# Kernel tuning notes

Measured on AMD Instinct MI355X. Metric: run time of the kernel, lower is better.

## Reference

```python
import jax, jax.numpy as jnp
import numpy as np

N = 50000          # nodes
E = 800000         # edges
IN = 32            # in_channels (train_tensor.shape[1])
OUT = 256          # out_channels
K = 4              # Chebyshev order
LAMBDA_MAX = 2.0   # canonical lambda_max for sym-normalized Laplacian


def setup_inputs() -> dict:
    key = jax.random.key(0)
    ks = jax.random.split(key, 32)
    inp = {}
    inp["X"] = jax.random.normal(ks[0], (N, IN), jnp.float32)
    inp["edge_index"] = jax.random.randint(ks[1], (2, E), 0, N)
    inp["edge_weight"] = jax.random.uniform(ks[2], (E,), jnp.float32)
    inp["H"] = jax.random.normal(ks[3], (N, OUT), jnp.float32)
    inp["C"] = jax.random.normal(ks[4], (N, OUT), jnp.float32)
    i = 5
    s_in = float(np.sqrt(6.0 / (IN + OUT)))   # glorot for W_g
    s_ch = float(np.sqrt(1.0 / OUT))          # ChebConv linear init scale
    for g in ["i", "f", "c", "o"]:
        inp[f"W_{g}"] = jax.random.uniform(ks[i], (IN, OUT), jnp.float32, -s_in, s_in); i += 1
        inp[f"b_{g}"] = jnp.zeros((1, OUT), jnp.float32)
        inp[f"conv_{g}_w"] = jax.random.uniform(ks[i], (K, OUT, OUT), jnp.float32, -s_ch, s_ch); i += 1
        inp[f"conv_{g}_b"] = jnp.zeros((OUT,), jnp.float32)
    return inp


def _cheb_basis(H, edge_index, edge_weight, lam):
    """Chebyshev basis T_0(L~)H .. T_{K-1}(L~)H for the scaled sym Laplacian.
    L~ = (2/lam) * (I - D^{-1/2} A D^{-1/2}) - I  (PyG ChebConv.__norm__)."""
    n = H.shape[0]
    src, dst = edge_index[0], edge_index[1]
    deg = jax.ops.segment_sum(edge_weight, src, num_segments=n)
    dis = jnp.where(deg > 0, jax.lax.rsqrt(deg), 0.0)
    w = -(2.0 / lam) * dis[src] * edge_weight * dis[dst]   # scaled off-diagonal
    d = 2.0 / lam - 1.0                                     # scaled diagonal

    def prop(x):  # L~ @ x via edge scatter + diagonal
        return jax.ops.segment_sum(w[:, None] * x[src], dst, num_segments=n) + d * x

    Tx0 = H
    Tx1 = prop(Tx0)
    Tx2 = 2.0 * prop(Tx1) - Tx0
    Tx3 = 2.0 * prop(Tx2) - Tx1
    return jnp.stack([Tx0, Tx1, Tx2, Tx3])  # [K, N, OUT]


def reference(X, edge_index, edge_weight, H, C,
              W_i, b_i, conv_i_w, conv_i_b,
              W_f, b_f, conv_f_w, conv_f_b,
              W_c, b_c, conv_c_w, conv_c_b,
              W_o, b_o, conv_o_w, conv_o_b):
    # Shared Chebyshev basis of H (identical across the 4 gates)
    Tx = _cheb_basis(H, edge_index, edge_weight, LAMBDA_MAX)  # [K, N, OUT]

    def gate(Wg, bg, cw, cb):
        conv = jnp.einsum('knf,kfo->no', Tx, cw) + cb
        return X @ Wg + conv + bg

    I = jax.nn.sigmoid(gate(W_i, b_i, conv_i_w, conv_i_b))
    F = jax.nn.sigmoid(gate(W_f, b_f, conv_f_w, conv_f_b))
    T = jnp.tanh(gate(W_c, b_c, conv_c_w, conv_c_b))
    C_new = F * C + I * T
    O = jax.nn.sigmoid(gate(W_o, b_o, conv_o_w, conv_o_b))
    H_new = O * jnp.tanh(C_new)
    return (H_new, C_new)
```

## Files before the change

kernel.cpp:

```cpp
#include <hip/hip_runtime.h>
#include <math.h>

#define NN   50000
#define EE   800000
#define INC  32
#define OUTC 256
#define NKB  132

using bf16x8 = __attribute__((ext_vector_type(8))) short;
using u16x8  = __attribute__((ext_vector_type(8))) unsigned short;
using f32x4  = __attribute__((ext_vector_type(4))) float;

struct __align__(8) Edge { int s; float w; };

__device__ __forceinline__ unsigned short f2b(float f) {
  union { float f; unsigned u; } v; v.f = f;
  return (unsigned short)((v.u + 0x7FFFu + ((v.u >> 16) & 1u)) >> 16);
}
__device__ __forceinline__ float b2f(unsigned short u) {
  union { unsigned u; float f; } v; v.u = ((unsigned)u) << 16; return v.f;
}


__global__ void k_edge1(const int* __restrict__ ei, const float* __restrict__ ew,
                        float* __restrict__ deg, int* __restrict__ cnt) {
  for (int e = blockIdx.x * blockDim.x + threadIdx.x; e < EE;
       e += gridDim.x * blockDim.x) {
    atomicAdd(&deg[ei[e]], ew[e]);
    atomicAdd(&cnt[ei[EE + e]], 1);
  }
}

__global__ __launch_bounds__(512) void k_scan1(const int* __restrict__ cnt,
                                               int* __restrict__ row_ptr,
                                               int* __restrict__ bsum) {
  __shared__ int sd[512];
  int t = threadIdx.x;
  int i = blockIdx.x * 512 + t;
  int x = (i < NN) ? cnt[i] : 0;
  sd[t] = x;
  __syncthreads();
  for (int off = 1; off < 512; off <<= 1) {
    int v = (t >= off) ? sd[t - off] : 0;
    __syncthreads();
    sd[t] += v;
    __syncthreads();
  }
  if (i < NN) row_ptr[i] = sd[t] - x;
  if (t == 511) bsum[blockIdx.x] = sd[511];
}

__global__ __launch_bounds__(128) void k_scan2(int* __restrict__ bsum,
                                               int* __restrict__ row_ptr,
                                               int nblk) {
  __shared__ int sd[128];
  int t = threadIdx.x;
  int x = (t < nblk) ? bsum[t] : 0;
  sd[t] = x;
  __syncthreads();
  for (int off = 1; off < 128; off <<= 1) {
    int v = (t >= off) ? sd[t - off] : 0;
    __syncthreads();
    sd[t] += v;
    __syncthreads();
  }
  if (t < nblk) bsum[t] = sd[t] - x;
  if (t == 127) row_ptr[NN] = sd[127];
}

__global__ void k_scan3(int* __restrict__ row_ptr, const int* __restrict__ bsum,
                        int* __restrict__ nxt, float* __restrict__ deg) {
  int i = blockIdx.x * blockDim.x + threadIdx.x;
  if (i < NN) {
    int v = row_ptr[i] + bsum[i >> 9];
    row_ptr[i] = v;
    nxt[i] = v;
    float d = deg[i];
    deg[i] = d > 0.f ? rsqrtf(d) : 0.f;
  }
}

__global__ void k_fill(const int* __restrict__ ei, const float* __restrict__ ew,
                       const float* __restrict__ dis, int* __restrict__ nxt,
                       Edge* __restrict__ ev) {
  for (int e = blockIdx.x * blockDim.x + threadIdx.x; e < EE;
       e += gridDim.x * blockDim.x) {
    int s = ei[e], d = ei[EE + e];
    int pos = atomicAdd(&nxt[d], 1);
    Edge eg; eg.s = s; eg.w = -dis[s] * ew[e] * dis[d];
    ev[pos] = eg;
  }
}


__global__ __launch_bounds__(256) void k_prop_bf(
    const int* __restrict__ row_ptr, const Edge* __restrict__ ev,
    const unsigned short* __restrict__ xb,
    const unsigned short* __restrict__ initb, float scale,
    unsigned short* __restrict__ outb, unsigned short* __restrict__ apk) {
  int wid = blockIdx.x * 4 + (threadIdx.x >> 6);
  if (wid >= NN) return;
  int lane = threadIdx.x & 63;
  int half = lane >> 5;
  int cl = lane & 31;
  int start = __builtin_amdgcn_readfirstlane(row_ptr[wid]);
  int end = __builtin_amdgcn_readfirstlane(row_ptr[wid + 1]);
  const size_t cofs = (size_t)(cl << 3);

  float a0[8], a1[8], a2[8], a3[8];
#pragma unroll
  for (int i = 0; i < 8; ++i) { a0[i] = 0.f; a1[i] = 0.f; a2[i] = 0.f; a3[i] = 0.f; }

  int j = start;
  for (; j + 7 < end; j += 8) {
    Edge e0 = ev[j + half];
    Edge e1 = ev[j + 2 + half];
    Edge e2 = ev[j + 4 + half];
    Edge e3 = ev[j + 6 + half];
    u16x8 u0 = *(const u16x8*)(xb + (size_t)e0.s * OUTC + cofs);
    u16x8 u1 = *(const u16x8*)(xb + (size_t)e1.s * OUTC + cofs);
    u16x8 u2 = *(const u16x8*)(xb + (size_t)e2.s * OUTC + cofs);
    u16x8 u3 = *(const u16x8*)(xb + (size_t)e3.s * OUTC + cofs);
#pragma unroll
    for (int i = 0; i < 8; ++i) {
      a0[i] = fmaf(e0.w, b2f(u0[i]), a0[i]);
      a1[i] = fmaf(e1.w, b2f(u1[i]), a1[i]);
      a2[i] = fmaf(e2.w, b2f(u2[i]), a2[i]);
      a3[i] = fmaf(e3.w, b2f(u3[i]), a3[i]);
    }
  }
  for (; j + 1 < end; j += 2) {
    Edge e0 = ev[j + half];
    u16x8 u0 = *(const u16x8*)(xb + (size_t)e0.s * OUTC + cofs);
#pragma unroll
    for (int i = 0; i < 8; ++i) a0[i] = fmaf(e0.w, b2f(u0[i]), a0[i]);
  }
  if (j < end) {
    Edge e0 = ev[j];
    float wv = half ? 0.f : e0.w;
    u16x8 u0 = *(const u16x8*)(xb + (size_t)e0.s * OUTC + cofs);
#pragma unroll
    for (int i = 0; i < 8; ++i) a0[i] = fmaf(wv, b2f(u0[i]), a0[i]);
  }

  float o[8];
#pragma unroll
  for (int i = 0; i < 8; ++i) {
    float s = (a0[i] + a1[i]) + (a2[i] + a3[i]);
    s += __shfl_xor(s, 32);
    o[i] = s;
  }
  if (initb) {
    u16x8 iv = *(const u16x8*)(initb + (size_t)wid * OUTC + cofs);
#pragma unroll
    for (int i = 0; i < 8; ++i) o[i] = scale * o[i] - b2f(iv[i]);
  }
  u16x8 h;
#pragma unroll
  for (int i = 0; i < 8; ++i) h[i] = f2b(o[i]);
  if (half == 0) {
    *(u16x8*)(apk + ((size_t)cl * NN + wid) * 8) = h;
  } else if (outb) {
    *(u16x8*)(outb + (size_t)wid * OUTC + cofs) = h;
  }
}


__global__ void k_packXH(const float* __restrict__ X, const float* __restrict__ H,
                         unsigned short* __restrict__ apk,
                         unsigned short* __restrict__ hrm) {
  int t = blockIdx.x * blockDim.x + threadIdx.x;
  if (t < NN * 4) {
    int row = t >> 2, kb = t & 3;
    float4 a = *(const float4*)(X + (size_t)row * INC + kb * 8);
    float4 b = *(const float4*)(X + (size_t)row * INC + kb * 8 + 4);
    u16x8 h;
    h[0] = f2b(a.x); h[1] = f2b(a.y); h[2] = f2b(a.z); h[3] = f2b(a.w);
    h[4] = f2b(b.x); h[5] = f2b(b.y); h[6] = f2b(b.z); h[7] = f2b(b.w);
    *(u16x8*)(apk + ((size_t)kb * NN + row) * 8) = h;
  } else if (t < NN * 36) {
    int u = t - NN * 4;
    int row = u >> 5, kb = u & 31;
    float4 a = *(const float4*)(H + (size_t)row * OUTC + kb * 8);
    float4 b = *(const float4*)(H + (size_t)row * OUTC + kb * 8 + 4);
    u16x8 h;
    h[0] = f2b(a.x); h[1] = f2b(a.y); h[2] = f2b(a.z); h[3] = f2b(a.w);
    h[4] = f2b(b.x); h[5] = f2b(b.y); h[6] = f2b(b.z); h[7] = f2b(b.w);
    *(u16x8*)(apk + ((size_t)(kb + 4) * NN + row) * 8) = h;
    *(u16x8*)(hrm + (size_t)row * OUTC + kb * 8) = h;
  }
}

struct BPtrs {
  const float* W[4];
  const float* cw[4];
  const float* b[4];
  const float* cb[4];
};

__global__ void k_packB(BPtrs bp, unsigned short* __restrict__ bpk,
                        float* __restrict__ bias_pk) {
  int t = blockIdx.x * blockDim.x + threadIdx.x;
  if (t >= NKB * 1024) return;
  int kb = t >> 10, p = t & 1023;
  int j = p >> 7, c = (p >> 6) & 1, g = (p >> 4) & 3, s = p & 15;
  int o = j * 32 + c * 16 + s;
  u16x8 h;
#pragma unroll
  for (int j8 = 0; j8 < 8; ++j8) {
    int k = kb * 8 + j8;
    float v = (k < 32) ? bp.W[g][k * OUTC + o]
                       : bp.cw[g][(size_t)(k - 32) * OUTC + o];
    h[j8] = f2b(v);
  }
  *(u16x8*)(bpk + (size_t)t * 8) = h;
  if (kb == 0) bias_pk[p] = bp.b[g][o] + bp.cb[g][o];
}


__device__ __forceinline__ float sigf(float x) {
  return __builtin_amdgcn_rcpf(1.0f + __expf(-x));
}
__device__ __forceinline__ float tanhfast(float x) {
  float e = __expf(2.0f * x);
  return 1.0f - 2.0f * __builtin_amdgcn_rcpf(e + 1.0f);
}

#define AS1(p) ((__attribute__((address_space(1))) void*)(p))
#define AS3(p) ((__attribute__((address_space(3))) void*)(p))

__global__ __launch_bounds__(512, 6) void k_gemm_mfma(
    const unsigned short* __restrict__ Apk,
    const unsigned short* __restrict__ Bpk,
    const float* __restrict__ bias_pk,
    const float* __restrict__ C,
    float* __restrict__ Hn, float* __restrict__ Cn) {
  __shared__ unsigned short Als[3][4 * 128 * 8];
  __shared__ unsigned short Bls[3][4 * 128 * 8];

  const int b = blockIdx.x;
  const int xcd = b & 7;
  const int slot = b >> 3;
  const int cgrp = slot & 7;
  const int rblk = xcd + ((slot >> 3) << 3);
  const int bm0 = rblk * 128;
  if (bm0 >= NN) return;
  const int cb0 = cgrp * 128;

  const int tid = threadIdx.x;
  const int lane = tid & 63;
  const int wid = tid >> 6;
  const int wr = wid >> 1;
  const int wc = wid & 1;

  f32x4 acc[2][4];
#pragma unroll
  for (int i = 0; i < 2; ++i)
#pragma unroll
    for (int j = 0; j < 4; ++j) acc[i][j] = (f32x4){0.f, 0.f, 0.f, 0.f};

  int a_row = bm0 + ((wid & 1) << 6) + lane;
  if (a_row > NN - 1) a_row = NN - 1;
  const unsigned short* aG = Apk + ((size_t)(wid >> 1) * NN + a_row) * 8;
  const int idxw = wid << 6;
  const unsigned short* bG =
      Bpk + (((size_t)(idxw >> 7)) * 1024 + cb0 + (idxw & 127) + lane) * 8;

  auto STAGE_A = [&](int buf, int tile) {
    __builtin_amdgcn_global_load_lds(AS1(aG + ((size_t)(tile << 2)) * NN * 8),
                                     AS3(&Als[buf][(wid << 6) * 8]), 16, 0, 0);
  };
  auto STAGE_B = [&](int buf, int tile) {
    __builtin_amdgcn_global_load_lds(AS1(bG + ((size_t)(tile << 2)) * 1024 * 8),
                                     AS3(&Bls[buf][(wid << 6) * 8]), 16, 0, 0);
  };

  const int koff = lane >> 4;
  const int r15 = lane & 15;
  const int NT = NKB / 4;

  STAGE_A(0, 0); STAGE_B(0, 0);
  STAGE_A(1, 1); STAGE_B(1, 1);
  int cur = 0;
  for (int t = 0; t < NT; ++t) {
    if (t < NT - 1)
      asm volatile("s_waitcnt vmcnt(2)\n\ts_barrier" ::: "memory");
    else
      asm volatile("s_waitcnt vmcnt(0)\n\ts_barrier" ::: "memory");

    const unsigned short* Ab = &Als[cur][((koff << 7) + (wr << 5) + r15) * 8];
    const unsigned short* Bb = &Bls[cur][((koff << 7) + (wc << 6) + r15) * 8];

    bf16x8 af0 = *(const bf16x8*)(Ab + 0 * 8);
    bf16x8 af1 = *(const bf16x8*)(Ab + 16 * 8);
    bf16x8 bf0 = *(const bf16x8*)(Bb + 0 * 8);
    bf16x8 bf1 = *(const bf16x8*)(Bb + 16 * 8);
    bf16x8 bf2 = *(const bf16x8*)(Bb + 32 * 8);
    bf16x8 bf3 = *(const bf16x8*)(Bb + 48 * 8);
    if (t + 2 < NT) { STAGE_A((t + 2) % 3, t + 2); STAGE_B((t + 2) % 3, t + 2); }
    __builtin_amdgcn_s_barrier();
    asm volatile("s_waitcnt lgkmcnt(0)" ::: "memory");
    __builtin_amdgcn_sched_barrier(0);
    __builtin_amdgcn_s_setprio(1);
    acc[0][0] = __builtin_amdgcn_mfma_f32_16x16x32_bf16(af0, bf0, acc[0][0], 0, 0, 0);
    acc[1][0] = __builtin_amdgcn_mfma_f32_16x16x32_bf16(af1, bf0, acc[1][0], 0, 0, 0);
    acc[0][1] = __builtin_amdgcn_mfma_f32_16x16x32_bf16(af0, bf1, acc[0][1], 0, 0, 0);
    acc[1][1] = __builtin_amdgcn_mfma_f32_16x16x32_bf16(af1, bf1, acc[1][1], 0, 0, 0);
    acc[0][2] = __builtin_amdgcn_mfma_f32_16x16x32_bf16(af0, bf2, acc[0][2], 0, 0, 0);
    acc[1][2] = __builtin_amdgcn_mfma_f32_16x16x32_bf16(af1, bf2, acc[1][2], 0, 0, 0);
    acc[0][3] = __builtin_amdgcn_mfma_f32_16x16x32_bf16(af0, bf3, acc[0][3], 0, 0, 0);
    acc[1][3] = __builtin_amdgcn_mfma_f32_16x16x32_bf16(af1, bf3, acc[1][3], 0, 0, 0);
    __builtin_amdgcn_s_setprio(0);

    cur = (cur + 1 == 3) ? 0 : cur + 1;
  }

  const int ocol = cgrp * 32 + (wc << 4) + r15;
  float bz[4];
#pragma unroll
  for (int g = 0; g < 4; ++g) bz[g] = bias_pk[cb0 + (wc << 6) + (g << 4) + r15];

#pragma unroll
  for (int mi = 0; mi < 2; ++mi) {
    int rowb = bm0 + (wr << 5) + (mi << 4) + ((lane >> 4) << 2);
#pragma unroll
    for (int q = 0; q < 4; ++q) {
      int r = rowb + q;
      if (r >= NN) continue;
      float zi = acc[mi][0][q] + bz[0];
      float zf = acc[mi][1][q] + bz[1];
      float zc = acc[mi][2][q] + bz[2];
      float zo = acc[mi][3][q] + bz[3];
      float cold = C[(size_t)r * OUTC + ocol];
      float I = sigf(zi), F = sigf(zf), T = tanhfast(zc), O = sigf(zo);
      float cn = fmaf(F, cold, I * T);
      Cn[(size_t)r * OUTC + ocol] = cn;
      Hn[(size_t)r * OUTC + ocol] = O * tanhfast(cn);
    }
  }
}


extern "C" void kernel_launch(void* const* d_in, const int* in_sizes, int n_in,
                              void* d_out, int out_size, void* d_ws, size_t ws_size,
                              hipStream_t stream) {
  const float* X = (const float*)d_in[0];
  const int* EI = (const int*)d_in[1];
  const float* EW = (const float*)d_in[2];
  const float* H = (const float*)d_in[3];
  const float* C = (const float*)d_in[4];

  char* ws = (char*)d_ws;
  size_t off = 0;
  auto alloc = [&](size_t bytes) -> void* {
    void* p = ws + off;
    off += (bytes + 255) & ~(size_t)255;
    return p;
  };
  int* row_ptr = (int*)alloc((NN + 1) * sizeof(int));
  int* cnt = (int*)alloc(NN * sizeof(int));
  int* nextp = (int*)alloc(NN * sizeof(int));
  int* bsum = (int*)alloc(128 * sizeof(int));
  Edge* ev = (Edge*)alloc(EE * sizeof(Edge));
  float* dis = (float*)alloc(NN * sizeof(float));
  unsigned short* Hrm = (unsigned short*)alloc((size_t)NN * OUTC * sizeof(unsigned short));
  unsigned short* T1rm = (unsigned short*)alloc((size_t)NN * OUTC * sizeof(unsigned short));
  unsigned short* T2rm = (unsigned short*)alloc((size_t)NN * OUTC * sizeof(unsigned short));
  unsigned short* Apk = (unsigned short*)alloc((size_t)NKB * NN * 8 * sizeof(unsigned short));
  unsigned short* Bpk = (unsigned short*)alloc((size_t)NKB * 1024 * 8 * sizeof(unsigned short));
  float* bias_pk = (float*)alloc(1024 * sizeof(float));
  (void)ws_size; (void)in_sizes; (void)n_in; (void)out_size;

  hipMemsetAsync(dis, 0, NN * sizeof(float), stream);
  hipMemsetAsync(cnt, 0, NN * sizeof(int), stream);

  const int ge = 1024;
  k_edge1<<<ge, 256, 0, stream>>>(EI, EW, dis, cnt);
  const int nscb = (NN + 511) / 512;
  k_scan1<<<nscb, 512, 0, stream>>>(cnt, row_ptr, bsum);
  k_scan2<<<1, 128, 0, stream>>>(bsum, row_ptr, nscb);
  k_scan3<<<(NN + 255) / 256, 256, 0, stream>>>(row_ptr, bsum, nextp, dis);
  k_fill<<<ge, 256, 0, stream>>>(EI, EW, dis, nextp, ev);

  k_packXH<<<(NN * 36 + 255) / 256, 256, 0, stream>>>(X, H, Apk, Hrm);
  BPtrs bp;
  for (int g = 0; g < 4; ++g) {
    bp.W[g] = (const float*)d_in[5 + 4 * g];
    bp.b[g] = (const float*)d_in[6 + 4 * g];
    bp.cw[g] = (const float*)d_in[7 + 4 * g];
    bp.cb[g] = (const float*)d_in[8 + 4 * g];
  }
  k_packB<<<(NKB * 1024 + 255) / 256, 256, 0, stream>>>(bp, Bpk, bias_pk);

  const int pgrid = (NN + 3) / 4;
  k_prop_bf<<<pgrid, 256, 0, stream>>>(row_ptr, ev, Hrm, nullptr, 1.f,
                                       T1rm, Apk + (size_t)36 * NN * 8);
  k_prop_bf<<<pgrid, 256, 0, stream>>>(row_ptr, ev, T1rm, Hrm, 2.f,
                                       T2rm, Apk + (size_t)68 * NN * 8);
  k_prop_bf<<<pgrid, 256, 0, stream>>>(row_ptr, ev, T2rm, T1rm, 2.f,
                                       nullptr, Apk + (size_t)100 * NN * 8);

  float* Hn = (float*)d_out;
  float* Cn = (float*)d_out + (size_t)NN * OUTC;
  k_gemm_mfma<<<8 * 49 * 8, 512, 0, stream>>>(Apk, Bpk, bias_pk, C, Hn, Cn);
}
```

Baseline: 495.4 us.

## Enlarge GEMM block tile to 128x256 with 4 waves and 4x8 MFMA accumulators

Restructures the fused gate GEMM so each 256-thread block computes a 128-row by 256-column tile, with each wave holding a 64x128 output (4x8 MFMA accumulators) instead of 32x64. Column groups drop from 8 to 4 per row block, so the A operand is re-read from global memory half as often and each LDS fragment feeds more MFMAs. The cost is many more accumulator registers per thread, lower occupancy (launch bounds 256,2), a larger LDS B buffer, and more loads in flight per stage, with vmcnt adjusted to match.

```diff
diff --git a/kernel.cpp b/kernel.cpp
--- a/kernel.cpp
+++ b/kernel.cpp
@@ -229,23 +229,23 @@
 #define AS1(p) ((__attribute__((address_space(1))) void*)(p))
 #define AS3(p) ((__attribute__((address_space(3))) void*)(p))
 
-__global__ __launch_bounds__(512, 6) void k_gemm_mfma(
+__global__ __launch_bounds__(256, 2) void k_gemm_mfma(
     const unsigned short* __restrict__ Apk,
     const unsigned short* __restrict__ Bpk,
     const float* __restrict__ bias_pk,
     const float* __restrict__ C,
     float* __restrict__ Hn, float* __restrict__ Cn) {
   __shared__ unsigned short Als[3][4 * 128 * 8];
-  __shared__ unsigned short Bls[3][4 * 128 * 8];
+  __shared__ unsigned short Bls[3][4 * 256 * 8];
 
   const int b = blockIdx.x;
   const int xcd = b & 7;
   const int slot = b >> 3;
-  const int cgrp = slot & 7;
-  const int rblk = xcd + ((slot >> 3) << 3);
+  const int cgrp = slot & 3;
+  const int rblk = xcd + ((slot >> 2) << 3);
   const int bm0 = rblk * 128;
   if (bm0 >= NN) return;
-  const int cb0 = cgrp * 128;
+  const int cb0 = cgrp * 256;
 
   const int tid = threadIdx.x;
   const int lane = tid & 63;
@@ -253,26 +253,32 @@
   const int wr = wid >> 1;
   const int wc = wid & 1;
 
-  f32x4 acc[2][4];
-#pragma unroll
-  for (int i = 0; i < 2; ++i)
-#pragma unroll
-    for (int j = 0; j < 4; ++j) acc[i][j] = (f32x4){0.f, 0.f, 0.f, 0.f};
+  f32x4 acc[4][8];
+#pragma unroll
+  for (int i = 0; i < 4; ++i)
+#pragma unroll
+    for (int j = 0; j < 8; ++j) acc[i][j] = (f32x4){0.f, 0.f, 0.f, 0.f};
 
   int a_row = bm0 + ((wid & 1) << 6) + lane;
   if (a_row > NN - 1) a_row = NN - 1;
-  const unsigned short* aG = Apk + ((size_t)(wid >> 1) * NN + a_row) * 8;
-  const int idxw = wid << 6;
-  const unsigned short* bG =
-      Bpk + (((size_t)(idxw >> 7)) * 1024 + cb0 + (idxw & 127) + lane) * 8;
+  const unsigned short* aG0 = Apk + ((size_t)(wid >> 1) * NN + a_row) * 8;
+  const unsigned short* aG1 = Apk + ((size_t)((wid >> 1) + 2) * NN + a_row) * 8;
+  const unsigned short* bG = Bpk + ((size_t)cb0 + (wid << 6) + lane) * 8;
 
   auto STAGE_A = [&](int buf, int tile) {
-    __builtin_amdgcn_global_load_lds(AS1(aG + ((size_t)(tile << 2)) * NN * 8),
+    const size_t kofs = (size_t)(tile << 2) * NN * 8;
+    __builtin_amdgcn_global_load_lds(AS1(aG0 + kofs),
                                      AS3(&Als[buf][(wid << 6) * 8]), 16, 0, 0);
+    __builtin_amdgcn_global_load_lds(AS1(aG1 + kofs),
+                                     AS3(&Als[buf][(256 + (wid << 6)) * 8]), 16, 0, 0);
   };
   auto STAGE_B = [&](int buf, int tile) {
-    __builtin_amdgcn_global_load_lds(AS1(bG + ((size_t)(tile << 2)) * 1024 * 8),
-                                     AS3(&Bls[buf][(wid << 6) * 8]), 16, 0, 0);
+#pragma unroll
+    for (int j = 0; j < 4; ++j) {
+      __builtin_amdgcn_global_load_lds(
+          AS1(bG + (((size_t)(tile << 2) + j) * 1024) * 8),
+          AS3(&Bls[buf][(j * 256 + (wid << 6)) * 8]), 16, 0, 0);
+    }
   };
 
   const int koff = lane >> 4;
@@ -284,58 +290,79 @@
   int cur = 0;
   for (int t = 0; t < NT; ++t) {
     if (t < NT - 1)
-      asm volatile("s_waitcnt vmcnt(2)\n\ts_barrier" ::: "memory");
+      asm volatile("s_waitcnt vmcnt(6)\n\ts_barrier" ::: "memory");
     else
       asm volatile("s_waitcnt vmcnt(0)\n\ts_barrier" ::: "memory");
 
-    const unsigned short* Ab = &Als[cur][((koff << 7) + (wr << 5) + r15) * 8];
-    const unsigned short* Bb = &Bls[cur][((koff << 7) + (wc << 6) + r15) * 8];
+    const unsigned short* Ab = &Als[cur][((koff << 7) + (wr << 6) + r15) * 8];
+    const unsigned short* Bb = &Bls[cur][((koff << 8) + (wc << 7) + r15) * 8];
 
     bf16x8 af0 = *(const bf16x8*)(Ab + 0 * 8);
     bf16x8 af1 = *(const bf16x8*)(Ab + 16 * 8);
+    bf16x8 af2 = *(const bf16x8*)(Ab + 32 * 8);
+    bf16x8 af3 = *(const bf16x8*)(Ab + 48 * 8);
     bf16x8 bf0 = *(const bf16x8*)(Bb + 0 * 8);
     bf16x8 bf1 = *(const bf16x8*)(Bb + 16 * 8);
     bf16x8 bf2 = *(const bf16x8*)(Bb + 32 * 8);
     bf16x8 bf3 = *(const bf16x8*)(Bb + 48 * 8);
+    bf16x8 bf4 = *(const bf16x8*)(Bb + 64 * 8);
+    bf16x8 bf5 = *(const bf16x8*)(Bb + 80 * 8);
+    bf16x8 bf6 = *(const bf16x8*)(Bb + 96 * 8);
+    bf16x8 bf7 = *(const bf16x8*)(Bb + 112 * 8);
     if (t + 2 < NT) { STAGE_A((t + 2) % 3, t + 2); STAGE_B((t + 2) % 3, t + 2); }
     __builtin_amdgcn_s_barrier();
     asm volatile("s_waitcnt lgkmcnt(0)" ::: "memory");
     __builtin_amdgcn_sched_barrier(0);
     __builtin_amdgcn_s_setprio(1);
-    acc[0][0] = __builtin_amdgcn_mfma_f32_16x16x32_bf16(af0, bf0, acc[0][0], 0, 0, 0);
-    acc[1][0] = __builtin_amdgcn_mfma_f32_16x16x32_bf16(af1, bf0, acc[1][0], 0, 0, 0);
-    acc[0][1] = __builtin_amdgcn_mfma_f32_16x16x32_bf16(af0, bf1, acc[0][1], 0, 0, 0);
-    acc[1][1] = __builtin_amdgcn_mfma_f32_16x16x32_bf16(af1, bf1, acc[1][1], 0, 0, 0);
-    acc[0][2] = __builtin_amdgcn_mfma_f32_16x16x32_bf16(af0, bf2, acc[0][2], 0, 0, 0);
-    acc[1][2] = __builtin_amdgcn_mfma_f32_16x16x32_bf16(af1, bf2, acc[1][2], 0, 0, 0);
-    acc[0][3] = __builtin_amdgcn_mfma_f32_16x16x32_bf16(af0, bf3, acc[0][3], 0, 0, 0);
-    acc[1][3] = __builtin_amdgcn_mfma_f32_16x16x32_bf16(af1, bf3, acc[1][3], 0, 0, 0);
+#define MM(m, n, bfn) acc[m][n] = __builtin_amdgcn_mfma_f32_16x16x32_bf16(af##m, bfn, acc[m][n], 0, 0, 0)
+    MM(0, 0, bf0); MM(1, 0, bf0); MM(2, 0, bf0); MM(3, 0, bf0);
+    MM(0, 1, bf1); MM(1, 1, bf1); MM(2, 1, bf1); MM(3, 1, bf1);
+    MM(0, 2, bf2); MM(1, 2, bf2); MM(2, 2, bf2); MM(3, 2, bf2);
+    MM(0, 3, bf3); MM(1, 3, bf3); MM(2, 3, bf3); MM(3, 3, bf3);
+    MM(0, 4, bf4); MM(1, 4, bf4); MM(2, 4, bf4); MM(3, 4, bf4);
+    MM(0, 5, bf5); MM(1, 5, bf5); MM(2, 5, bf5); MM(3, 5, bf5);
+    MM(0, 6, bf6); MM(1, 6, bf6); MM(2, 6, bf6); MM(3, 6, bf6);
+    MM(0, 7, bf7); MM(1, 7, bf7); MM(2, 7, bf7); MM(3, 7, bf7);
+#undef MM
     __builtin_amdgcn_s_setprio(0);
 
     cur = (cur + 1 == 3) ? 0 : cur + 1;
   }
 
-  const int ocol = cgrp * 32 + (wc << 4) + r15;
-  float bz[4];
-#pragma unroll
-  for (int g = 0; g < 4; ++g) bz[g] = bias_pk[cb0 + (wc << 6) + (g << 4) + r15];
-
-#pragma unroll
-  for (int mi = 0; mi < 2; ++mi) {
-    int rowb = bm0 + (wr << 5) + (mi << 4) + ((lane >> 4) << 2);
+  const int ocb = (cgrp * 2 + wc) * 32 + r15;
+  float bz[8];
+#pragma unroll
+  for (int n = 0; n < 8; ++n) bz[n] = bias_pk[cb0 + (wc << 7) + (n << 4) + r15];
+
+#pragma unroll
+  for (int mi = 0; mi < 4; ++mi) {
+    int rowb = bm0 + (wr << 6) + (mi << 4) + ((lane >> 4) << 2);
 #pragma unroll
     for (int q = 0; q < 4; ++q) {
       int r = rowb + q;
       if (r >= NN) continue;
-      float zi = acc[mi][0][q] + bz[0];
-      float zf = acc[mi][1][q] + bz[1];
-      float zc = acc[mi][2][q] + bz[2];
-      float zo = acc[mi][3][q] + bz[3];
-      float cold = C[(size_t)r * OUTC + ocol];
-      float I = sigf(zi), F = sigf(zf), T = tanhfast(zc), O = sigf(zo);
-      float cn = fmaf(F, cold, I * T);
-      Cn[(size_t)r * OUTC + ocol] = cn;
-      Hn[(size_t)r * OUTC + ocol] = O * tanhfast(cn);
+      {
+        float zi = acc[mi][0][q] + bz[0];
+        float zf = acc[mi][1][q] + bz[1];
+        float zc = acc[mi][2][q] + bz[2];
+        float zo = acc[mi][3][q] + bz[3];
+        float cold = C[(size_t)r * OUTC + ocb];
+        float I = sigf(zi), F = sigf(zf), T = tanhfast(zc), O = sigf(zo);
+        float cn = fmaf(F, cold, I * T);
+        Cn[(size_t)r * OUTC + ocb] = cn;
+        Hn[(size_t)r * OUTC + ocb] = O * tanhfast(cn);
+      }
+      {
+        float zi = acc[mi][4][q] + bz[4];
+        float zf = acc[mi][5][q] + bz[5];
+        float zc = acc[mi][6][q] + bz[6];
+        float zo = acc[mi][7][q] + bz[7];
+        float cold = C[(size_t)r * OUTC + ocb + 16];
+        float I = sigf(zi), F = sigf(zf), T = tanhfast(zc), O = sigf(zo);
+        float cn = fmaf(F, cold, I * T);
+        Cn[(size_t)r * OUTC + ocb + 16] = cn;
+        Hn[(size_t)r * OUTC + ocb + 16] = O * tanhfast(cn);
+      }
     }
   }
 }
@@ -402,5 +429,5 @@
 
   float* Hn = (float*)d_out;
   float* Cn = (float*)d_out + (size_t)NN * OUTC;
-  k_gemm_mfma<<<8 * 49 * 8, 512, 0, stream>>>(Apk, Bpk, bias_pk, C, Hn, Cn);
-}
+  k_gemm_mfma<<<8 * 49 * 4, 256, 0, stream>>>(Apk, Bpk, bias_pk, C, Hn, Cn);
+}
```

After: 504.1 us. Within noise of the previous version (+1.8%).

## Read GEMM A operand directly from row-major basis buffers instead of packed copy

Applied to the files above, without the earlier changes.

Removes the separate k-block-packed A matrix. The propagation and pack kernels now write only row-major bf16 tensors (X, H, T1, T2, T3), and the GEMM stages A tiles straight from these buffers by selecting the source per k-tile. This drops the duplicate writes of every basis tensor into the packed layout. In exchange the GEMM's A loads become strided row accesses of 16 bytes per lane instead of contiguous packed reads, which may hurt coalescing.

```diff
diff --git a/kernel.cpp b/kernel.cpp
--- a/kernel.cpp
+++ b/kernel.cpp
@@ -97,7 +97,7 @@
     const int* __restrict__ row_ptr, const Edge* __restrict__ ev,
     const unsigned short* __restrict__ xb,
     const unsigned short* __restrict__ initb, float scale,
-    unsigned short* __restrict__ outb, unsigned short* __restrict__ apk) {
+    unsigned short* __restrict__ outb) {
   int wid = blockIdx.x * 4 + (threadIdx.x >> 6);
   if (wid >= NN) return;
   int lane = threadIdx.x & 63;
@@ -155,19 +155,17 @@
 #pragma unroll
     for (int i = 0; i < 8; ++i) o[i] = scale * o[i] - b2f(iv[i]);
   }
-  u16x8 h;
-#pragma unroll
-  for (int i = 0; i < 8; ++i) h[i] = f2b(o[i]);
-  if (half == 0) {
-    *(u16x8*)(apk + ((size_t)cl * NN + wid) * 8) = h;
-  } else if (outb) {
+  if (half == 1) {
+    u16x8 h;
+#pragma unroll
+    for (int i = 0; i < 8; ++i) h[i] = f2b(o[i]);
     *(u16x8*)(outb + (size_t)wid * OUTC + cofs) = h;
   }
 }
 
 
 __global__ void k_packXH(const float* __restrict__ X, const float* __restrict__ H,
-                         unsigned short* __restrict__ apk,
+                         unsigned short* __restrict__ xrm,
                          unsigned short* __restrict__ hrm) {
   int t = blockIdx.x * blockDim.x + threadIdx.x;
   if (t < NN * 4) {
@@ -177,7 +175,7 @@
     u16x8 h;
     h[0] = f2b(a.x); h[1] = f2b(a.y); h[2] = f2b(a.z); h[3] = f2b(a.w);
     h[4] = f2b(b.x); h[5] = f2b(b.y); h[6] = f2b(b.z); h[7] = f2b(b.w);
-    *(u16x8*)(apk + ((size_t)kb * NN + row) * 8) = h;
+    *(u16x8*)(xrm + (size_t)row * INC + kb * 8) = h;
   } else if (t < NN * 36) {
     int u = t - NN * 4;
     int row = u >> 5, kb = u & 31;
@@ -186,7 +184,6 @@
     u16x8 h;
     h[0] = f2b(a.x); h[1] = f2b(a.y); h[2] = f2b(a.z); h[3] = f2b(a.w);
     h[4] = f2b(b.x); h[5] = f2b(b.y); h[6] = f2b(b.z); h[7] = f2b(b.w);
-    *(u16x8*)(apk + ((size_t)(kb + 4) * NN + row) * 8) = h;
     *(u16x8*)(hrm + (size_t)row * OUTC + kb * 8) = h;
   }
 }
@@ -230,7 +227,11 @@
 #define AS3(p) ((__attribute__((address_space(3))) void*)(p))
 
 __global__ __launch_bounds__(512, 6) void k_gemm_mfma(
-    const unsigned short* __restrict__ Apk,
+    const unsigned short* __restrict__ Xrm,
+    const unsigned short* __restrict__ Hrm,
+    const unsigned short* __restrict__ T1rm,
+    const unsigned short* __restrict__ T2rm,
+    const unsigned short* __restrict__ T3rm,
     const unsigned short* __restrict__ Bpk,
     const float* __restrict__ bias_pk,
     const float* __restrict__ C,
@@ -261,13 +262,21 @@
 
   int a_row = bm0 + ((wid & 1) << 6) + lane;
   if (a_row > NN - 1) a_row = NN - 1;
-  const unsigned short* aG = Apk + ((size_t)(wid >> 1) * NN + a_row) * 8;
+  const size_t rowX = (size_t)a_row * INC;
+  const size_t row256 = (size_t)a_row * OUTC;
+  const int kbl8 = (wid >> 1) << 3;
   const int idxw = wid << 6;
   const unsigned short* bG =
       Bpk + (((size_t)(idxw >> 7)) * 1024 + cb0 + (idxw & 127) + lane) * 8;
 
   auto STAGE_A = [&](int buf, int tile) {
-    __builtin_amdgcn_global_load_lds(AS1(aG + ((size_t)(tile << 2)) * NN * 8),
+    const unsigned short* src;
+    if (tile == 0)      src = Xrm + rowX;
+    else if (tile < 9)  src = Hrm  + row256 + (size_t)(tile - 1) * 32;
+    else if (tile < 17) src = T1rm + row256 + (size_t)(tile - 9) * 32;
+    else if (tile < 25) src = T2rm + row256 + (size_t)(tile - 17) * 32;
+    else                src = T3rm + row256 + (size_t)(tile - 25) * 32;
+    __builtin_amdgcn_global_load_lds(AS1(src + kbl8),
                                      AS3(&Als[buf][(wid << 6) * 8]), 16, 0, 0);
   };
   auto STAGE_B = [&](int buf, int tile) {
@@ -363,10 +372,11 @@
   int* bsum = (int*)alloc(128 * sizeof(int));
   Edge* ev = (Edge*)alloc(EE * sizeof(Edge));
   float* dis = (float*)alloc(NN * sizeof(float));
+  unsigned short* Xrm = (unsigned short*)alloc((size_t)NN * INC * sizeof(unsigned short));
   unsigned short* Hrm = (unsigned short*)alloc((size_t)NN * OUTC * sizeof(unsigned short));
   unsigned short* T1rm = (unsigned short*)alloc((size_t)NN * OUTC * sizeof(unsigned short));
   unsigned short* T2rm = (unsigned short*)alloc((size_t)NN * OUTC * sizeof(unsigned short));
-  unsigned short* Apk = (unsigned short*)alloc((size_t)NKB * NN * 8 * sizeof(unsigned short));
+  unsigned short* T3rm = (unsigned short*)alloc((size_t)NN * OUTC * sizeof(unsigned short));
   unsigned short* Bpk = (unsigned short*)alloc((size_t)NKB * 1024 * 8 * sizeof(unsigned short));
   float* bias_pk = (float*)alloc(1024 * sizeof(float));
   (void)ws_size; (void)in_sizes; (void)n_in; (void)out_size;
@@ -382,7 +392,7 @@
   k_scan3<<<(NN + 255) / 256, 256, 0, stream>>>(row_ptr, bsum, nextp, dis);
   k_fill<<<ge, 256, 0, stream>>>(EI, EW, dis, nextp, ev);
 
-  k_packXH<<<(NN * 36 + 255) / 256, 256, 0, stream>>>(X, H, Apk, Hrm);
+  k_packXH<<<(NN * 36 + 255) / 256, 256, 0, stream>>>(X, H, Xrm, Hrm);
   BPtrs bp;
   for (int g = 0; g < 4; ++g) {
     bp.W[g] = (const float*)d_in[5 + 4 * g];
@@ -393,14 +403,12 @@
   k_packB<<<(NKB * 1024 + 255) / 256, 256, 0, stream>>>(bp, Bpk, bias_pk);
 
   const int pgrid = (NN + 3) / 4;
-  k_prop_bf<<<pgrid, 256, 0, stream>>>(row_ptr, ev, Hrm, nullptr, 1.f,
-                                       T1rm, Apk + (size_t)36 * NN * 8);
-  k_prop_bf<<<pgrid, 256, 0, stream>>>(row_ptr, ev, T1rm, Hrm, 2.f,
-                                       T2rm, Apk + (size_t)68 * NN * 8);
-  k_prop_bf<<<pgrid, 256, 0, stream>>>(row_ptr, ev, T2rm, T1rm, 2.f,
-                                       nullptr, Apk + (size_t)100 * NN * 8);
+  k_prop_bf<<<pgrid, 256, 0, stream>>>(row_ptr, ev, Hrm, nullptr, 1.f, T1rm);
+  k_prop_bf<<<pgrid, 256, 0, stream>>>(row_ptr, ev, T1rm, Hrm, 2.f, T2rm);
+  k_prop_bf<<<pgrid, 256, 0, stream>>>(row_ptr, ev, T2rm, T1rm, 2.f, T3rm);
 
   float* Hn = (float*)d_out;
   float* Cn = (float*)d_out + (size_t)NN * OUTC;
-  k_gemm_mfma<<<8 * 49 * 8, 512, 0, stream>>>(Apk, Bpk, bias_pk, C, Hn, Cn);
-}
+  k_gemm_mfma<<<8 * 49 * 8, 512, 0, stream>>>(Xrm, Hrm, T1rm, T2rm, T3rm,
+                                              Bpk, bias_pk, C, Hn, Cn);
+}
```

After: 545.3 us. 1.1x slower.
